# Optimization experiments

Measured on AMD Instinct MI355X. Metric: run time of the kernel, lower is better.

## Reference

```python
import jax, jax.numpy as jnp
import numpy as np

B, T, C = 4, 2048, 1024
H = 16
D = C // H  # head_dim = 64

def setup_inputs() -> dict:
    key = jax.random.key(0)
    k1, k2, k3 = jax.random.split(key, 3)
    x = jax.random.normal(k1, (B, T, C), dtype=jnp.float32)
    w_qkv = jax.random.normal(k2, (C, 3 * C), dtype=jnp.float32) * (1.0 / np.sqrt(C))
    w_proj = jax.random.normal(k3, (C, C), dtype=jnp.float32) * (1.0 / np.sqrt(C))
    return {"x": x, "w_qkv": w_qkv, "w_proj": w_proj}

def reference(x, w_qkv, w_proj):
    Bq, Tq, Cq = x.shape
    qkv = x @ w_qkv                                   # [B,T,3C]
    q, k, v = jnp.split(qkv, 3, axis=2)
    # [B,T,C] -> [B,H,T,D]
    q = q.reshape(Bq, Tq, H, D).transpose(0, 2, 1, 3)
    k = k.reshape(Bq, Tq, H, D).transpose(0, 2, 1, 3)
    v = v.reshape(Bq, Tq, H, D).transpose(0, 2, 1, 3)
    att = jnp.einsum('bhqd,bhkd->bhqk', q, k) / jnp.sqrt(jnp.float32(D))
    causal = jnp.tril(jnp.ones((Tq, Tq), dtype=bool))
    att = jnp.where(causal[None, None], att, jnp.float32(-jnp.inf))
    att = jax.nn.softmax(att, axis=-1)
    y = jnp.einsum('bhqk,bhkd->bhqd', att, v)         # [B,H,T,D]
    y = y.transpose(0, 2, 1, 3).reshape(Bq, Tq, Cq)
    return y @ w_proj
```

## Files before the change

### kernel.cpp

```cpp
#include <hip/hip_runtime.h>

typedef unsigned short u16;
typedef __attribute__((ext_vector_type(8))) short s16x8;
typedef __attribute__((ext_vector_type(4))) float f32x4;
typedef __attribute__((ext_vector_type(16))) float f32x16;

#define MFMA(a, b, c) __builtin_amdgcn_mfma_f32_16x16x32_bf16((a), (b), (c), 0, 0, 0)
#define MFMA32(a, b, c) __builtin_amdgcn_mfma_f32_32x32x16_bf16((a), (b), (c), 0, 0, 0)

#define LDS16(gp, lp)                                                          \
  __builtin_amdgcn_global_load_lds(                                            \
      (__attribute__((address_space(1))) void*)(gp),                           \
      (__attribute__((address_space(3))) void*)(lp), 16, 0, 0)

#define WAITVM(n) asm volatile("s_waitcnt vmcnt(" #n ")" ::: "memory")

#if __has_builtin(__builtin_amdgcn_exp2f)
#define EXP2F(x) __builtin_amdgcn_exp2f(x)
#else
#define EXP2F(x) exp2f(x)
#endif
#if __has_builtin(__builtin_amdgcn_rcpf)
#define RCPF(x) __builtin_amdgcn_rcpf(x)
#else
#define RCPF(x) (1.0f / (x))
#endif

__device__ __forceinline__ u16 f2bf(float f) {
  unsigned u = __float_as_uint(f);
  u += 0x7fffu + ((u >> 16) & 1u);
  return (u16)(u >> 16);
}

__device__ __forceinline__ int cvtpk(float a, float b) {
  int r;
  asm("v_cvt_pk_bf16_f32 %0, %1, %2" : "=v"(r) : "v"(a), "v"(b));
  return r;
}

__global__ void cast_x_kernel(const float* __restrict__ in, u16* __restrict__ out) {
  const int idx = (blockIdx.x * 256 + threadIdx.x) * 4;
  const float4 v = *(const float4*)(in + idx);
  ushort4 o;
  o.x = f2bf(v.x); o.y = f2bf(v.y); o.z = f2bf(v.z); o.w = f2bf(v.w);
  *(ushort4*)(out + idx) = o;
}

__global__ void transpose_cast(const float* __restrict__ in, u16* __restrict__ out,
                               int Kd, int Nd) {
  __shared__ float t[64][65];
  const int tid = threadIdx.x;
  const int nb = blockIdx.x * 64, kb = blockIdx.y * 64;
#pragma unroll
  for (int it = 0; it < 4; it++) {
    const int flat = it * 1024 + tid * 4;
    const int rr = flat >> 6, cc = flat & 63;
    const float4 v = *(const float4*)(in + (size_t)(kb + rr) * Nd + nb + cc);
    t[rr][cc] = v.x; t[rr][cc + 1] = v.y; t[rr][cc + 2] = v.z; t[rr][cc + 3] = v.w;
  }
  __syncthreads();
#pragma unroll
  for (int it = 0; it < 4; it++) {
    const int flat = it * 1024 + tid * 4;
    const int rn = flat >> 6, ck = flat & 63;
    ushort4 o;
    o.x = f2bf(t[ck][rn]);     o.y = f2bf(t[ck + 1][rn]);
    o.z = f2bf(t[ck + 2][rn]); o.w = f2bf(t[ck + 3][rn]);
    *(ushort4*)(out + (size_t)(nb + rn) * Kd + kb + ck) = o;
  }
}

template <int EPI>
__global__ __launch_bounds__(512, 2)
void gemm256(const u16* __restrict__ A, const u16* __restrict__ Bt,
             float* __restrict__ Cout, int Ndim,
             u16* __restrict__ qp, u16* __restrict__ kp, u16* __restrict__ vp) {
  __shared__ alignas(16) u16 L[4 * 12288];
  const int tid = threadIdx.x;
  const int lane = tid & 63, wid = tid >> 6;
  const int r = lane & 15, qq = lane >> 4;
  const int wr = wid >> 1, wc = wid & 1;
  const int gx = gridDim.x;
  const int nwg = gx * gridDim.y;
  const int bid = blockIdx.x + gx * blockIdx.y;
  const int swz = (bid & 7) * (nwg >> 3) + (bid >> 3);
  const int tn = (swz % gx) * 128, tm = (swz / gx) * 256;

  f32x4 acc[4][4];
#pragma unroll
  for (int i = 0; i < 4; i++)
#pragma unroll
    for (int j = 0; j < 4; j++) acc[i][j] = (f32x4){0.f, 0.f, 0.f, 0.f};

  const u16* gA = A + (size_t)(tm + (tid & 255)) * 1024 + (tid >> 8) * 8;
  const u16* gB = Bt + (size_t)(tn + (tid & 127)) * 1024 + (tid >> 7) * 8;
  const int la0 = tid * 8, la1 = (tid + 512) * 8, lb0 = 8192 + tid * 8;

#define GSTAGE(b, t)                                                \
  do {                                                              \
    const u16* ga_ = gA + (t) * 32;                                 \
    u16* lp_ = L + (b) * 12288;                                     \
    LDS16(ga_, lp_ + la0);                                          \
    LDS16(ga_ + 16, lp_ + la1);                                     \
    LDS16(gB + (t) * 32, lp_ + lb0);                                \
  } while (0)

  const int arow = wr * 64 + r, brow = wc * 64 + r;
  const int aoff = qq * 2048 + arow * 8;
  const int boff = 8192 + qq * 1024 + brow * 8;

#define GCOMPUTE(b)                                                 \
  do {                                                              \
    const u16* lp_ = L + (b) * 12288;                               \
    s16x8 af[4], bfv[4];                                            \
    _Pragma("unroll")                                               \
    for (int f = 0; f < 4; f++)                                     \
      af[f] = *(const s16x8*)(lp_ + aoff + f * 128);                \
    _Pragma("unroll")                                               \
    for (int f = 0; f < 4; f++)                                     \
      bfv[f] = *(const s16x8*)(lp_ + boff + f * 128);               \
    __builtin_amdgcn_s_setprio(1);                                  \
    _Pragma("unroll")                                               \
    for (int fm = 0; fm < 4; fm++)                                  \
      _Pragma("unroll")                                             \
      for (int fn = 0; fn < 4; fn++)                                \
        acc[fm][fn] = MFMA(af[fm], bfv[fn], acc[fm][fn]);           \
    __builtin_amdgcn_s_setprio(0);                                  \
  } while (0)

  GSTAGE(0, 0);
  GSTAGE(1, 1);
  GSTAGE(2, 2);
  for (int kt = 0; kt < 30; kt++) {
    WAITVM(6);
    __builtin_amdgcn_s_barrier();
    if (kt < 29) GSTAGE((kt + 3) & 3, kt + 3);
    GCOMPUTE(kt & 3);
  }
  WAITVM(3);
  __builtin_amdgcn_s_barrier();
  GCOMPUTE(2);
  WAITVM(0);
  __builtin_amdgcn_s_barrier();
  GCOMPUTE(3);
#undef GSTAGE
#undef GCOMPUTE

  if (EPI == 0) {
#pragma unroll
    for (int fm = 0; fm < 4; fm++) {
#pragma unroll
      for (int j2 = 0; j2 < 4; j2++) {
        const int mm = tm + wr * 64 + fm * 16 + qq * 4 + j2;
        const int bb = mm >> 11, tt = mm & 2047;
#pragma unroll
        for (int fn = 0; fn < 4; fn++) {
          const int n = tn + wc * 64 + fn * 16 + r;
          const u16 bv = f2bf(acc[fm][fn][j2]);
          const int which = n >> 10;
          const int hh = (n >> 6) & 15, dd = n & 63;
          const int bhh = bb * 16 + hh;
          if (which == 0)      qp[((size_t)bhh * 2048 + tt) * 64 + dd] = bv;
          else if (which == 1) kp[((size_t)bhh * 2048 + tt) * 64 + dd] = bv;
          else                 vp[((size_t)bhh * 64 + dd) * 2048 + tt] = bv;
        }
      }
    }
  } else {
#pragma unroll
    for (int fm = 0; fm < 4; fm++) {
#pragma unroll
      for (int j2 = 0; j2 < 4; j2++) {
        const int mm = tm + wr * 64 + fm * 16 + qq * 4 + j2;
#pragma unroll
        for (int fn = 0; fn < 4; fn++) {
          const int n = tn + wc * 64 + fn * 16 + r;
          Cout[(size_t)mm * Ndim + n] = acc[fm][fn][j2];
        }
      }
    }
  }
}

__global__ __launch_bounds__(256, 2)
void attn_fwd(const u16* __restrict__ qg, const u16* __restrict__ kg,
              const u16* __restrict__ vtg, u16* __restrict__ yg) {
  __shared__ alignas(16) u16 Kl[2][64 * 64];
  __shared__ alignas(16) u16 Vl[2][64 * 64];
  const int tid = threadIdx.x;
  const int w = tid >> 6, lane = tid & 63;
  const int q5 = lane & 31, hi = lane >> 5;
  const int bh = blockIdx.x;
  const int qi = (int)(gridDim.y - 1 - blockIdx.y);
  const int qb = qi * 128;
  const int qrow = qb + w * 32 + q5;
  const float C = 0.18033688011112042f;

  const u16* qbase = qg + ((size_t)bh * 2048 + qrow) * 64;
  s16x8 qf[4];
#pragma unroll
  for (int ks = 0; ks < 4; ks++)
    qf[ks] = *(const s16x8*)(qbase + ks * 16 + hi * 8);

  const int c0 = tid, c1 = tid + 256;
  const int r0 = c0 >> 3, s0 = (c0 & 7) ^ (r0 & 7);
  const int r1 = c1 >> 3, s1 = (c1 & 7) ^ (r1 & 7);
  const u16* kga = kg + ((size_t)bh * 2048 + r0) * 64 + s0 * 8;
  const u16* kgb = kg + ((size_t)bh * 2048 + r1) * 64 + s1 * 8;
  const u16* vga = vtg + ((size_t)bh * 64 + r0) * 2048 + s0 * 8;
  const u16* vgb = vtg + ((size_t)bh * 64 + r1) * 2048 + s1 * 8;

  f32x16 ya, yb;
#pragma unroll
  for (int r = 0; r < 16; r++) { ya[r] = 0.f; yb[r] = 0.f; }
  float m_run = -3.0e38f, l_run = 0.f;

  const int nt = qb / 64 + 2;

#define STAGE(b, t)                                               \
  do {                                                            \
    LDS16(kga + (size_t)(t) * 4096, Kl[b] + c0 * 8);              \
    LDS16(kgb + (size_t)(t) * 4096, Kl[b] + c1 * 8);              \
    LDS16(vga + (size_t)(t) * 64,   Vl[b] + c0 * 8);              \
    LDS16(vgb + (size_t)(t) * 64,   Vl[b] + c1 * 8);              \
  } while (0)

  STAGE(0, 0);
  __syncthreads();

  for (int t = 0; t < nt; t++) {
    const int buf = t & 1;
    if (t + 1 < nt) STAGE(buf ^ 1, t + 1);
    const int kv0 = t * 64;
    const u16* Kb = Kl[buf];
    const u16* Vb = Vl[buf];

    if (kv0 <= qb + w * 32 + 31) {
      f32x16 sa, sb;
#pragma unroll
      for (int r = 0; r < 16; r++) { sa[r] = 0.f; sb[r] = 0.f; }
      __builtin_amdgcn_s_setprio(1);
#pragma unroll
      for (int ks = 0; ks < 4; ks++) {
        const int slot = ((ks * 2 + hi) ^ (lane & 7)) * 8;
        const s16x8 ka  = *(const s16x8*)(Kb + q5 * 64 + slot);
        const s16x8 kb2 = *(const s16x8*)(Kb + (32 + q5) * 64 + slot);
        sa = MFMA32(ka, qf[ks], sa);
        sb = MFMA32(kb2, qf[ks], sb);
      }
      __builtin_amdgcn_s_setprio(0);

      s16x8 va[4], vb2[4];
#pragma unroll
      for (int ks4 = 0; ks4 < 4; ks4++) {
        const int sv = ((ks4 * 2 + hi) ^ (lane & 7)) * 8;
        va[ks4]  = *(const s16x8*)(Vb + q5 * 64 + sv);
        vb2[ks4] = *(const s16x8*)(Vb + (32 + q5) * 64 + sv);
      }

      if (kv0 + 63 > qb + w * 32) {
#pragma unroll
        for (int r = 0; r < 16; r++) {
          const int kl = kv0 + (r & 3) + 8 * (r >> 2) + 4 * hi;
          if (kl > qrow)      sa[r] = -3.0e38f;
          if (kl + 32 > qrow) sb[r] = -3.0e38f;
        }
      }

      float mx0 = -3.0e38f, mx1 = -3.0e38f, mx2 = -3.0e38f, mx3 = -3.0e38f;
#pragma unroll
      for (int r = 0; r < 16; r += 4) {
        mx0 = fmaxf(mx0, fmaxf(sa[r], sb[r]));
        mx1 = fmaxf(mx1, fmaxf(sa[r + 1], sb[r + 1]));
        mx2 = fmaxf(mx2, fmaxf(sa[r + 2], sb[r + 2]));
        mx3 = fmaxf(mx3, fmaxf(sa[r + 3], sb[r + 3]));
      }
      float mx = fmaxf(fmaxf(mx0, mx1), fmaxf(mx2, mx3));
      mx = fmaxf(mx, __shfl_xor(mx, 32));
      const float mxs = mx * C;

      if (!__all(mxs - m_run <= 8.0f)) {
        const float m2 = fmaxf(m_run, mxs);
        const float alpha = EXP2F(m_run - m2);
        m_run = m2;
        l_run *= alpha;
#pragma unroll
        for (int r = 0; r < 16; r++) { ya[r] *= alpha; yb[r] *= alpha; }
      }

      const float nm2 = -m_run;
      float ls0 = 0.f, ls1 = 0.f, ls2 = 0.f, ls3 = 0.f;
#pragma unroll
      for (int r = 0; r < 16; r += 4) {
        float p;
        p = EXP2F(fmaf(sa[r], C, nm2));     sa[r] = p;     ls0 += p;
        p = EXP2F(fmaf(sa[r + 1], C, nm2)); sa[r + 1] = p; ls1 += p;
        p = EXP2F(fmaf(sa[r + 2], C, nm2)); sa[r + 2] = p; ls2 += p;
        p = EXP2F(fmaf(sa[r + 3], C, nm2)); sa[r + 3] = p; ls3 += p;
        p = EXP2F(fmaf(sb[r], C, nm2));     sb[r] = p;     ls0 += p;
        p = EXP2F(fmaf(sb[r + 1], C, nm2)); sb[r + 1] = p; ls1 += p;
        p = EXP2F(fmaf(sb[r + 2], C, nm2)); sb[r + 2] = p; ls2 += p;
        p = EXP2F(fmaf(sb[r + 3], C, nm2)); sb[r + 3] = p; ls3 += p;
      }
      float ls = (ls0 + ls1) + (ls2 + ls3);
      ls += __shfl_xor(ls, 32);
      l_run += ls;

      s16x8 bfrag[4];
#pragma unroll
      for (int kb = 0; kb < 2; kb++) {
        const f32x16* pv = kb ? &sb : &sa;
        int wv[8], xv[8];
#pragma unroll
        for (int i = 0; i < 8; i++) wv[i] = cvtpk((*pv)[2 * i], (*pv)[2 * i + 1]);
#pragma unroll
        for (int i = 0; i < 8; i++) xv[i] = __shfl_xor(wv[i], 32);
        union { int4 i4; s16x8 s8; } u0, u1;
        u0.i4 = hi ? make_int4(xv[2], xv[3], wv[2], wv[3])
                   : make_int4(wv[0], wv[1], xv[0], xv[1]);
        u1.i4 = hi ? make_int4(xv[6], xv[7], wv[6], wv[7])
                   : make_int4(wv[4], wv[5], xv[4], xv[5]);
        bfrag[kb * 2]     = u0.s8;
        bfrag[kb * 2 + 1] = u1.s8;
      }

      __builtin_amdgcn_s_setprio(1);
#pragma unroll
      for (int ks4 = 0; ks4 < 4; ks4++) {
        ya = MFMA32(va[ks4], bfrag[ks4], ya);
        yb = MFMA32(vb2[ks4], bfrag[ks4], yb);
      }
      __builtin_amdgcn_s_setprio(0);
    }
    __syncthreads();
  }
#undef STAGE

  const float linv = RCPF(l_run);
  const int b = bh >> 4, h = bh & 15;
  u16* yrow = yg + ((size_t)b * 2048 + qrow) * 1024 + h * 64;
#pragma unroll
  for (int dt = 0; dt < 2; dt++) {
    const f32x16* Y = dt ? &yb : &ya;
#pragma unroll
    for (int p2 = 0; p2 < 8; p2++) {
      const int pk = cvtpk((*Y)[2 * p2] * linv, (*Y)[2 * p2 + 1] * linv);
      const int d0 = dt * 32 + (p2 >> 1) * 8 + hi * 4 + (p2 & 1) * 2;
      *reinterpret_cast<int*>(yrow + d0) = pk;
    }
  }
}

extern "C" void kernel_launch(void* const* d_in, const int* in_sizes, int n_in,
                              void* d_out, int out_size, void* d_ws, size_t ws_size,
                              hipStream_t stream) {
  const float* x = (const float*)d_in[0];
  const float* wqkv = (const float*)d_in[1];
  const float* wproj = (const float*)d_in[2];
  float* out = (float*)d_out;

  char* ws = (char*)d_ws;
  u16* xb     = (u16*)(ws);
  u16* wqkvT  = (u16*)(ws + 16777216);
  u16* wprojT = (u16*)(ws + 23068672);
  u16* qw     = (u16*)(ws + 25165824);
  u16* kw     = (u16*)(ws + 41943040);
  u16* vtw    = (u16*)(ws + 58720256);
  u16* yw     = (u16*)(ws + 75497472);
  (void)in_sizes; (void)n_in; (void)out_size; (void)ws_size;

  cast_x_kernel<<<8192, 256, 0, stream>>>(x, xb);
  transpose_cast<<<dim3(48, 16), 256, 0, stream>>>(wqkv, wqkvT, 1024, 3072);
  transpose_cast<<<dim3(16, 16), 256, 0, stream>>>(wproj, wprojT, 1024, 1024);
  gemm256<0><<<dim3(24, 32), 512, 0, stream>>>(xb, wqkvT, nullptr, 3072, qw, kw, vtw);
  attn_fwd<<<dim3(64, 16), 256, 0, stream>>>(qw, kw, vtw, yw);
  gemm256<1><<<dim3(8, 32), 512, 0, stream>>>(yw, wprojT, out, 1024,
                                              nullptr, nullptr, nullptr);
}
```

Before: 320.6 us.

## Restructure GEMM into triple-buffered LDS pipeline with higher occupancy bound

```diff
diff --git a/kernel.cpp b/kernel.cpp
--- a/kernel.cpp
+++ b/kernel.cpp
@@ -71,15 +71,16 @@
 }
 
 template <int EPI>
-__global__ __launch_bounds__(512, 2)
-void gemm256(const u16* __restrict__ A, const u16* __restrict__ Bt,
-             float* __restrict__ Cout, int Ndim,
-             u16* __restrict__ qp, u16* __restrict__ kp, u16* __restrict__ vp) {
-  __shared__ alignas(16) u16 L[4 * 12288];
+__global__ __launch_bounds__(512, 4)
+void gemmp(const u16* __restrict__ A, const u16* __restrict__ Bt,
+           float* __restrict__ Cout, int Ndim,
+           u16* __restrict__ qp, u16* __restrict__ kp, u16* __restrict__ vp) {
+  __shared__ alignas(16) u16 L[3 * 12288];
   const int tid = threadIdx.x;
-  const int lane = tid & 63, wid = tid >> 6;
+  const int lane = tid & 63;
+  const int wid = tid >> 6;
   const int r = lane & 15, qq = lane >> 4;
-  const int wr = wid >> 1, wc = wid & 1;
+  const int wm = wid >> 1, wn = wid & 1;
   const int gx = gridDim.x;
   const int nwg = gx * gridDim.y;
   const int bid = blockIdx.x + gx * blockIdx.y;
@@ -94,31 +95,32 @@
 
   const u16* gA = A + (size_t)(tm + (tid & 255)) * 1024 + (tid >> 8) * 8;
   const u16* gB = Bt + (size_t)(tn + (tid & 127)) * 1024 + (tid >> 7) * 8;
-  const int la0 = tid * 8, la1 = (tid + 512) * 8, lb0 = 8192 + tid * 8;
-
-#define GSTAGE(b, t)                                                \
+  const int la0 = tid * 8, la1 = tid * 8 + 4096, lb0 = 8192 + tid * 8;
+
+#define GSTAGE(bb, t)                                               \
   do {                                                              \
-    const u16* ga_ = gA + (t) * 32;                                 \
-    u16* lp_ = L + (b) * 12288;                                     \
-    LDS16(ga_, lp_ + la0);                                          \
-    LDS16(ga_ + 16, lp_ + la1);                                     \
-    LDS16(gB + (t) * 32, lp_ + lb0);                                \
+    const u16* sa_ = gA + (size_t)(t) * 32;                         \
+    u16* lp_ = L + (bb);                                            \
+    LDS16(sa_, lp_ + la0);                                          \
+    LDS16(sa_ + 16, lp_ + la1);                                     \
+    LDS16(gB + (size_t)(t) * 32, lp_ + lb0);                        \
   } while (0)
 
-  const int arow = wr * 64 + r, brow = wc * 64 + r;
-  const int aoff = qq * 2048 + arow * 8;
-  const int boff = 8192 + qq * 1024 + brow * 8;
-
-#define GCOMPUTE(b)                                                 \
+  const int aoff = qq * 2048 + (wm * 64 + r) * 8;
+  const int boff = 8192 + qq * 1024 + (wn * 64 + r) * 8;
+
+#define GPHASE(t, DO_STAGE, LAST)                                   \
   do {                                                              \
-    const u16* lp_ = L + (b) * 12288;                               \
+    const int bb_ = ((t) % 3) * 12288;                              \
     s16x8 af[4], bfv[4];                                            \
     _Pragma("unroll")                                               \
     for (int f = 0; f < 4; f++)                                     \
-      af[f] = *(const s16x8*)(lp_ + aoff + f * 128);                \
+      af[f] = *(const s16x8*)(L + bb_ + aoff + f * 128);            \
     _Pragma("unroll")                                               \
     for (int f = 0; f < 4; f++)                                     \
-      bfv[f] = *(const s16x8*)(lp_ + boff + f * 128);               \
+      bfv[f] = *(const s16x8*)(L + bb_ + boff + f * 128);           \
+    if (DO_STAGE) GSTAGE((((t) + 2) % 3) * 12288, (t) + 2);         \
+    __builtin_amdgcn_s_barrier();                                   \
     __builtin_amdgcn_s_setprio(1);                                  \
     _Pragma("unroll")                                               \
     for (int fm = 0; fm < 4; fm++)                                  \
@@ -126,36 +128,49 @@
       for (int fn = 0; fn < 4; fn++)                                \
         acc[fm][fn] = MFMA(af[fm], bfv[fn], acc[fm][fn]);           \
     __builtin_amdgcn_s_setprio(0);                                  \
+    if (!(LAST)) __builtin_amdgcn_s_barrier();                      \
   } while (0)
 
   GSTAGE(0, 0);
-  GSTAGE(1, 1);
-  GSTAGE(2, 2);
-  for (int kt = 0; kt < 30; kt++) {
-    WAITVM(6);
-    __builtin_amdgcn_s_barrier();
-    if (kt < 29) GSTAGE((kt + 3) & 3, kt + 3);
-    GCOMPUTE(kt & 3);
-  }
+  GSTAGE(12288, 1);
   WAITVM(3);
   __builtin_amdgcn_s_barrier();
-  GCOMPUTE(2);
-  WAITVM(0);
-  __builtin_amdgcn_s_barrier();
-  GCOMPUTE(3);
+  for (int t = 0; t < 30; t++) {
+    const int bb_ = (t % 3) * 12288;
+    s16x8 af[4], bfv[4];
+#pragma unroll
+    for (int f = 0; f < 4; f++)
+      af[f] = *(const s16x8*)(L + bb_ + aoff + f * 128);
+#pragma unroll
+    for (int f = 0; f < 4; f++)
+      bfv[f] = *(const s16x8*)(L + bb_ + boff + f * 128);
+    GSTAGE(((t + 2) % 3) * 12288, t + 2);
+    __builtin_amdgcn_s_barrier();
+    __builtin_amdgcn_s_setprio(1);
+#pragma unroll
+    for (int fm = 0; fm < 4; fm++)
+#pragma unroll
+      for (int fn = 0; fn < 4; fn++)
+        acc[fm][fn] = MFMA(af[fm], bfv[fn], acc[fm][fn]);
+    __builtin_amdgcn_s_setprio(0);
+    if (t < 29) WAITVM(3); else WAITVM(0);
+    __builtin_amdgcn_s_barrier();
+  }
+  GPHASE(30, 0, 0);
+  GPHASE(31, 0, 1);
 #undef GSTAGE
-#undef GCOMPUTE
+#undef GPHASE
 
   if (EPI == 0) {
 #pragma unroll
     for (int fm = 0; fm < 4; fm++) {
 #pragma unroll
       for (int j2 = 0; j2 < 4; j2++) {
-        const int mm = tm + wr * 64 + fm * 16 + qq * 4 + j2;
+        const int mm = tm + wm * 64 + fm * 16 + qq * 4 + j2;
         const int bb = mm >> 11, tt = mm & 2047;
 #pragma unroll
         for (int fn = 0; fn < 4; fn++) {
-          const int n = tn + wc * 64 + fn * 16 + r;
+          const int n = tn + wn * 64 + fn * 16 + r;
           const u16 bv = f2bf(acc[fm][fn][j2]);
           const int which = n >> 10;
           const int hh = (n >> 6) & 15, dd = n & 63;
@@ -171,10 +186,10 @@
     for (int fm = 0; fm < 4; fm++) {
 #pragma unroll
       for (int j2 = 0; j2 < 4; j2++) {
-        const int mm = tm + wr * 64 + fm * 16 + qq * 4 + j2;
+        const int mm = tm + wm * 64 + fm * 16 + qq * 4 + j2;
 #pragma unroll
         for (int fn = 0; fn < 4; fn++) {
-          const int n = tn + wc * 64 + fn * 16 + r;
+          const int n = tn + wn * 64 + fn * 16 + r;
           Cout[(size_t)mm * Ndim + n] = acc[fm][fn][j2];
         }
       }
@@ -372,8 +387,8 @@
   cast_x_kernel<<<8192, 256, 0, stream>>>(x, xb);
   transpose_cast<<<dim3(48, 16), 256, 0, stream>>>(wqkv, wqkvT, 1024, 3072);
   transpose_cast<<<dim3(16, 16), 256, 0, stream>>>(wproj, wprojT, 1024, 1024);
-  gemm256<0><<<dim3(24, 32), 512, 0, stream>>>(xb, wqkvT, nullptr, 3072, qw, kw, vtw);
+  gemmp<0><<<dim3(24, 32), 512, 0, stream>>>(xb, wqkvT, nullptr, 3072, qw, kw, vtw);
   attn_fwd<<<dim3(64, 16), 256, 0, stream>>>(qw, kw, vtw, yw);
-  gemm256<1><<<dim3(8, 32), 512, 0, stream>>>(yw, wprojT, out, 1024,
-                                              nullptr, nullptr, nullptr);
-}
+  gemmp<1><<<dim3(8, 32), 512, 0, stream>>>(yw, wprojT, out, 1024,
+                                            nullptr, nullptr, nullptr);
+}
```

New measurement: 314.0 us. -2.1%, faster.
